# Optimization experiments

Hardware: AMD Instinct MI355X
Metric: run time of the kernel (lower is better)

## Reference

```python
import jax, jax.numpy as jnp
import numpy as np

D_MODEL, NHEAD, D_FF = 1024, 16, 4096
HEAD_DIM = D_MODEL // NHEAD
LN_EPS = 1e-5


def _layer_norm(x, g, b):
    m = jnp.mean(x, axis=-1, keepdims=True)
    v = jnp.var(x, axis=-1, keepdims=True)
    return (x - m) * jax.lax.rsqrt(v + LN_EPS) * g + b


def setup_inputs() -> dict:
    key = jax.random.key(0)
    ks = jax.random.split(key, 16)
    s = 0.02
    d = {
        "x": jax.random.normal(ks[0], (4, 2048, D_MODEL), dtype=jnp.float32),
        "wq": jax.random.normal(ks[1], (D_MODEL, D_MODEL), dtype=jnp.float32) * s,
        "bq": jnp.zeros((D_MODEL,), jnp.float32),
        "wk": jax.random.normal(ks[2], (D_MODEL, D_MODEL), dtype=jnp.float32) * s,
        "bk": jnp.zeros((D_MODEL,), jnp.float32),
        "wv": jax.random.normal(ks[3], (D_MODEL, D_MODEL), dtype=jnp.float32) * s,
        "bv": jnp.zeros((D_MODEL,), jnp.float32),
        "wo": jax.random.normal(ks[4], (D_MODEL, D_MODEL), dtype=jnp.float32) * s,
        "bo": jnp.zeros((D_MODEL,), jnp.float32),
        "ln1_g": jnp.ones((D_MODEL,), jnp.float32),
        "ln1_b": jnp.zeros((D_MODEL,), jnp.float32),
        "ln2_g": jnp.ones((D_MODEL,), jnp.float32),
        "ln2_b": jnp.zeros((D_MODEL,), jnp.float32),
        "w1": jax.random.normal(ks[5], (D_MODEL, D_FF), dtype=jnp.float32) * s,
        "b1": jnp.zeros((D_FF,), jnp.float32),
        "w2": jax.random.normal(ks[6], (D_FF, D_MODEL), dtype=jnp.float32) * s,
        "b2": jnp.zeros((D_MODEL,), jnp.float32),
        "wlr": jax.random.normal(ks[7], (D_MODEL, 1), dtype=jnp.float32) * s,
        "blr": jnp.zeros((1,), jnp.float32),
    }
    return d


def reference(x, wq, bq, wk, bk, wv, bv, wo, bo, ln1_g, ln1_b, ln2_g, ln2_b,
              w1, b1, w2, b2, wlr, blr):
    N, L, E = x.shape
    h, hd = NHEAD, HEAD_DIM

    # --- pre-LN self-attention ---
    xn = _layer_norm(x, ln1_g, ln1_b)
    q = (xn @ wq + bq).reshape(N, L, h, hd)
    k = (xn @ wk + bk).reshape(N, L, h, hd)
    v = (xn @ wv + bv).reshape(N, L, h, hd)
    scale = 1.0 / np.sqrt(hd).astype(np.float32)
    scores = jnp.einsum("nlhd,nshd->nhls", q, k) * scale  # [N,h,L,S]
    w = jax.nn.softmax(scores, axis=-1)
    attn = jnp.einsum("nhls,nshd->nlhd", w, v).reshape(N, L, E)
    x = x + (attn @ wo + bo)

    # --- pre-LN MLP (ReLU), dropout = identity in eval ---
    xn2 = _layer_norm(x, ln2_g, ln2_b)
    x = x + (jax.nn.relu(xn2 @ w1 + b1) @ w2 + b2)

    logits = x[:, 0] @ wlr + blr  # [N,1]
    half = logits.shape[0] // 2
    real, fake = logits[:half], logits[half:]
    # BCE-with-logits: target 1 -> softplus(-z); target 0 -> softplus(z)
    loss_real = jnp.mean(jax.nn.softplus(-real))
    loss_fake = jnp.mean(jax.nn.softplus(fake))
    loss = (loss_fake + loss_real) * 0.5
    return (x, loss, loss_fake)
```

## Files before the change

### kernel.cpp

```cpp
#include <hip/hip_runtime.h>

typedef float  float4v  __attribute__((ext_vector_type(4)));
typedef int    int4v    __attribute__((ext_vector_type(4)));
typedef unsigned short ushort4v __attribute__((ext_vector_type(4)));
typedef short  short4v  __attribute__((ext_vector_type(4)));
typedef __bf16 bf16x8   __attribute__((ext_vector_type(8)));
typedef __bf16 bf16x2   __attribute__((ext_vector_type(2)));

#define D_MODEL 1024
#define NHEAD   16
#define HEAD_DIM 64
#define D_FF    4096
#define SEQ     2048
#define NBATCH  4
#define NTOK    (SEQ*NBATCH)
#define QSTR    3072

#define SCL 0.18033688011112042f

__device__ __forceinline__ unsigned short f2bf(float f){
  __bf16 h = (__bf16)f;
  return __builtin_bit_cast(unsigned short, h);
}
__device__ __forceinline__ float bf2f(unsigned short h){
  unsigned int u = ((unsigned int)h) << 16;
  return __builtin_bit_cast(float, u);
}
__device__ __forceinline__ unsigned int pk2bf(float lo, float hi){
  bf16x2 v; v[0] = (__bf16)lo; v[1] = (__bf16)hi;
  return __builtin_bit_cast(unsigned int, v);
}

typedef const __attribute__((address_space(1))) void* as1cv;
typedef __attribute__((address_space(3))) void* as3v;
__device__ __forceinline__ void gl_lds16(const void* g, void* l){
  __builtin_amdgcn_global_load_lds((as1cv)(unsigned long long)g,
                                   (as3v)(unsigned int)(unsigned long long)l,
                                   16, 0, 0);
}

__global__ __launch_bounds__(256)
void transpose_bf16_k(const float* __restrict__ in, unsigned short* __restrict__ out,
                      int K, int N)
{
  __shared__ float t[32][33];
  const int n0 = blockIdx.x * 32, k0 = blockIdx.y * 32;
  const int tx = threadIdx.x & 31, ty = threadIdx.x >> 5;
  #pragma unroll
  for(int i=0;i<32;i+=8) t[ty+i][tx] = in[(long)(k0+ty+i)*N + n0 + tx];
  __syncthreads();
  #pragma unroll
  for(int i=0;i<32;i+=8) out[(long)(n0+ty+i)*K + k0 + tx] = f2bf(t[tx][ty+i]);
}

__global__ __launch_bounds__(256)
void concat_bias(const float* __restrict__ bq, const float* __restrict__ bk,
                 const float* __restrict__ bv, float* __restrict__ out)
{
  int i = blockIdx.x*256 + threadIdx.x;
  float v = (i < 1024) ? bq[i] : (i < 2048) ? bk[i-1024] : bv[i-2048];
  out[i] = v;
}

__global__ __launch_bounds__(256)
void transpose_v_head(const unsigned short* __restrict__ in,
                      unsigned short* __restrict__ out)
{
  __shared__ unsigned short t[64][72];
  const int s0 = blockIdx.x * 64, h = blockIdx.y, n = blockIdx.z;
  const int tid = threadIdx.x;
  #pragma unroll
  for(int i=0;i<2;i++){
    int id = i*256 + tid;
    int r = id >> 3, p = (id & 7) * 8;
    *(int4v*)&t[r][p] = *(const int4v*)&in[((long)(n*SEQ + s0 + r))*QSTR + h*HEAD_DIM + p];
  }
  __syncthreads();
  #pragma unroll
  for(int i=0;i<2;i++){
    int id = i*256 + tid;
    int d = id >> 3, p = (id & 7) * 8;
    ushort4v a, b;
    #pragma unroll
    for(int j=0;j<4;j++){ a[j] = t[p+j][d]; b[j] = t[p+4+j][d]; }
    unsigned short* dst = out + ((long)((n*NHEAD + h)*HEAD_DIM + d))*SEQ + s0 + p;
    *(ushort4v*)dst = a;
    *(ushort4v*)(dst+4) = b;
  }
}

__global__ __launch_bounds__(256)
void ln_bf16(const float* __restrict__ x, const float* __restrict__ g,
             const float* __restrict__ b, unsigned short* __restrict__ out)
{
  const int row = blockIdx.x, tid = threadIdx.x;
  const float* xr = x + (long)row * D_MODEL;
  float4v v = *(const float4v*)(xr + tid*4);
  float s = v[0]+v[1]+v[2]+v[3];
  float q = v[0]*v[0]+v[1]*v[1]+v[2]*v[2]+v[3]*v[3];
  #pragma unroll
  for(int off=32; off; off>>=1){ s += __shfl_down(s, off); q += __shfl_down(q, off); }
  __shared__ float sb[4], qb[4], stat[2];
  const int w = tid>>6, lane = tid&63;
  if(lane==0){ sb[w]=s; qb[w]=q; }
  __syncthreads();
  if(tid==0){
    float S = sb[0]+sb[1]+sb[2]+sb[3];
    float Q = qb[0]+qb[1]+qb[2]+qb[3];
    float mean = S * (1.0f/D_MODEL);
    float var  = Q * (1.0f/D_MODEL) - mean*mean;
    stat[0] = mean;
    stat[1] = rsqrtf(var + 1e-5f);
  }
  __syncthreads();
  const float mean = stat[0], rstd = stat[1];
  ushort4v o;
  #pragma unroll
  for(int i=0;i<4;i++){
    int c = tid*4 + i;
    o[i] = f2bf((v[i]-mean)*rstd*g[c] + b[c]);
  }
  *(ushort4v*)(out + (long)row*D_MODEL + tid*4) = o;
}

template<int EPI>
__global__ __launch_bounds__(256, 2)
void gemm_bf16(const unsigned short* __restrict__ A,
               const unsigned short* __restrict__ Bt,
               const float* __restrict__ bias,
               const float* __restrict__ res,
               void* __restrict__ Cout,
               int M, int N, int K)
{
  __shared__ unsigned short As[128][64];
  __shared__ unsigned short Bs[128][64];
  const int tid = threadIdx.x;
  const int bm = blockIdx.x, bn = blockIdx.y;
  const int lane = tid & 63, w = tid >> 6;
  const int wm = (w >> 1) * 64, wn = (w & 1) * 64;
  const int l15 = lane & 15, quad = lane >> 4;
  const int r8 = lane >> 3, c8 = lane & 7;
  const int swc = c8 ^ r8;

  float4v acc[4][4];
  #pragma unroll
  for(int i=0;i<4;i++)
    #pragma unroll
    for(int j=0;j<4;j++){ float4v z = {0.f,0.f,0.f,0.f}; acc[i][j] = z; }

  const unsigned short* Abase = A  + ((long)bm*128 + w*32 + r8)*K + swc*8;
  const unsigned short* Bbase = Bt + ((long)bn*128 + w*32 + r8)*K + swc*8;
  unsigned short* AsW = &As[w*32][0];
  unsigned short* BsW = &Bs[w*32][0];

  for(int k0 = 0; k0 < K; k0 += 64){
    __syncthreads();
    #pragma unroll
    for(int i=0;i<4;i++){
      gl_lds16(Abase + (long)i*8*K + k0, AsW + i*8*64);
      gl_lds16(Bbase + (long)i*8*K + k0, BsW + i*8*64);
    }
    __syncthreads();

    #pragma unroll
    for(int kh=0; kh<2; kh++){
      const int jsw = ((kh*4 + quad) ^ (l15 & 7)) * 8;
      bf16x8 af[4], bfr[4];
      #pragma unroll
      for(int i=0;i<4;i++){
        af[i]  = *(const bf16x8*)&As[wm + i*16 + l15][jsw];
        bfr[i] = *(const bf16x8*)&Bs[wn + i*16 + l15][jsw];
      }
      #pragma unroll
      for(int i=0;i<4;i++)
        #pragma unroll
        for(int j=0;j<4;j++)
          acc[i][j] = __builtin_amdgcn_mfma_f32_16x16x32_bf16(af[i], bfr[j], acc[i][j], 0, 0, 0);
    }
  }

  #pragma unroll
  for(int i=0;i<4;i++){
    #pragma unroll
    for(int r=0;r<4;r++){
      const int row = bm*128 + wm + i*16 + quad*4 + r;
      const long base = (long)row * N + bn*128 + wn;
      #pragma unroll
      for(int j=0;j<4;j++){
        const int ct = j*16 + l15;
        float val = acc[i][j][r] + bias[bn*128 + wn + ct];
        if constexpr (EPI == 1) val = fmaxf(val, 0.f);
        if constexpr (EPI == 2)
          ((float*)Cout)[base + ct] = val + res[base + ct];
        else
          ((unsigned short*)Cout)[base + ct] = f2bf(val);
      }
    }
  }
}

__global__ __launch_bounds__(256)
void attn_mfma(const unsigned short* __restrict__ qm,
               const unsigned short* __restrict__ km,
               const unsigned short* __restrict__ vt,
               unsigned short* __restrict__ om)
{
  __shared__ unsigned short Ks[2][128][64];
  __shared__ unsigned short Vs[2][64][128];

  const int tid = threadIdx.x;
  const int w = tid >> 6, lane = tid & 63;
  const int l15 = lane & 15, quad = lane >> 4;
  const int r8 = lane >> 3, c8 = lane & 7;
  const int swc = c8 ^ r8;
  const int h = blockIdx.y, n = blockIdx.z;
  const int qbase = blockIdx.x * 128 + w * 32;

  bf16x8 qf[2][2];
  #pragma unroll
  for(int g=0; g<2; g++)
    #pragma unroll
    for(int ds=0; ds<2; ds++)
      qf[g][ds] = *(const bf16x8*)(qm + ((long)(n*SEQ + qbase + g*16 + l15))*QSTR
                                      + h*HEAD_DIM + ds*32 + quad*8);

  const unsigned short* kstage = km + ((long)(n*SEQ + w*32 + r8))*QSTR + h*HEAD_DIM + swc*8;
  const unsigned short* vhead = vt + ((long)((n*NHEAD + h)*HEAD_DIM))*SEQ;
  const int vrow_off = (lane >> 4);
  const int vpos = lane & 15;

  float lsum[2] = {0.f, 0.f};
  float4v oacc[4][2];
  #pragma unroll
  for(int dt=0; dt<4; dt++)
    #pragma unroll
    for(int g=0; g<2; g++){ float4v z={0.f,0.f,0.f,0.f}; oacc[dt][g]=z; }

  {
    unsigned short* KsW = &Ks[0][w*32][0];
    #pragma unroll
    for(int i=0;i<4;i++)
      gl_lds16(kstage + (long)i*8*QSTR, KsW + i*8*64);
    #pragma unroll
    for(int i=0;i<4;i++){
      int vrow = w*16 + i*4 + vrow_off;
      gl_lds16(vhead + (long)vrow*SEQ + (vpos ^ (vrow & 7))*8,
               &Vs[0][w*16 + i*4][0]);
    }
  }
  __syncthreads();

  const int NT = SEQ/128;
  for(int t = 0; t < NT; t++){
    const int cur = t & 1;
    if(t + 1 < NT){
      const int s1 = (t+1)*128;
      unsigned short* KsW = &Ks[cur^1][w*32][0];
      const unsigned short* kn = kstage + (long)s1*QSTR;
      #pragma unroll
      for(int i=0;i<4;i++)
        gl_lds16(kn + (long)i*8*QSTR, KsW + i*8*64);
      #pragma unroll
      for(int i=0;i<4;i++){
        int vrow = w*16 + i*4 + vrow_off;
        gl_lds16(vhead + (long)vrow*SEQ + s1 + (vpos ^ (vrow & 7))*8,
                 &Vs[cur^1][w*16 + i*4][0]);
      }
    }

    #pragma unroll
    for(int c=0; c<8; c++){
      bf16x8 ka0 = *(const bf16x8*)&Ks[cur][c*16 + l15][((quad  ) ^ (l15 & 7))*8];
      bf16x8 ka1 = *(const bf16x8*)&Ks[cur][c*16 + l15][((quad+4) ^ (l15 & 7))*8];
      float4v s0a = {0.f,0.f,0.f,0.f}, s1a = {0.f,0.f,0.f,0.f};
      s0a = __builtin_amdgcn_mfma_f32_16x16x32_bf16(ka0, qf[0][0], s0a, 0,0,0);
      s0a = __builtin_amdgcn_mfma_f32_16x16x32_bf16(ka1, qf[0][1], s0a, 0,0,0);
      s1a = __builtin_amdgcn_mfma_f32_16x16x32_bf16(ka0, qf[1][0], s1a, 0,0,0);
      s1a = __builtin_amdgcn_mfma_f32_16x16x32_bf16(ka1, qf[1][1], s1a, 0,0,0);

      float p00 = exp2f(s0a[0]*SCL), p01 = exp2f(s0a[1]*SCL);
      float p02 = exp2f(s0a[2]*SCL), p03 = exp2f(s0a[3]*SCL);
      float p10 = exp2f(s1a[0]*SCL), p11 = exp2f(s1a[1]*SCL);
      float p12 = exp2f(s1a[2]*SCL), p13 = exp2f(s1a[3]*SCL);
      lsum[0] += (p00+p01)+(p02+p03);
      lsum[1] += (p10+p11)+(p12+p13);
      unsigned int pl0 = pk2bf(p00,p01), ph0 = pk2bf(p02,p03);
      unsigned int pl1 = pk2bf(p10,p11), ph1 = pk2bf(p12,p13);
      short4v pf0, pf1;
      pf0 = __builtin_bit_cast(short4v, (unsigned long long)pl0 | ((unsigned long long)ph0<<32));
      pf1 = __builtin_bit_cast(short4v, (unsigned long long)pl1 | ((unsigned long long)ph1<<32));

      const int cc = c*4 + quad;
      const int vcol = (((cc>>1) ^ (l15 & 7))*8 + (cc & 1)*4);
      #pragma unroll
      for(int dt=0; dt<4; dt++){
        ushort4v vu = *(const ushort4v*)&Vs[cur][dt*16 + l15][vcol];
        short4v vfr = __builtin_bit_cast(short4v, vu);
        oacc[dt][0] = __builtin_amdgcn_mfma_f32_16x16x16bf16_1k(vfr, pf0, oacc[dt][0], 0,0,0);
        oacc[dt][1] = __builtin_amdgcn_mfma_f32_16x16x16bf16_1k(vfr, pf1, oacc[dt][1], 0,0,0);
      }
    }
    __syncthreads();
  }

  #pragma unroll
  for(int g=0; g<2; g++){
    lsum[g] += __shfl_xor(lsum[g], 16);
    lsum[g] += __shfl_xor(lsum[g], 32);
  }
  float inv[2] = {1.f/lsum[0], 1.f/lsum[1]};

  unsigned short* Os = (unsigned short*)Ks + w*32*80;
  #pragma unroll
  for(int g=0; g<2; g++){
    #pragma unroll
    for(int dt=0; dt<4; dt++){
      unsigned int d0 = pk2bf(oacc[dt][g][0]*inv[g], oacc[dt][g][1]*inv[g]);
      unsigned int d1 = pk2bf(oacc[dt][g][2]*inv[g], oacc[dt][g][3]*inv[g]);
      unsigned int* dst = (unsigned int*)&Os[(g*16 + l15)*80 + dt*16 + quad*4];
      dst[0] = d0; dst[1] = d1;
    }
  }
  const int q = lane >> 1, half = lane & 1;
  unsigned short* orow = om + ((long)(n*SEQ + qbase + q))*D_MODEL + h*HEAD_DIM + half*32;
  #pragma unroll
  for(int j=0;j<4;j++){
    int4v vI = *(int4v*)&Os[q*80 + half*32 + j*8];
    *(int4v*)(orow + j*8) = vI;
  }
}

__global__ __launch_bounds__(256)
void loss_k(const float* __restrict__ xo, const float* __restrict__ wlr,
            const float* __restrict__ blr, float* __restrict__ out)
{
  const int tid = threadIdx.x, w = tid>>6, lane = tid&63;
  const float* row = xo + (long)w * SEQ * D_MODEL;
  float s = 0.f;
  for(int c=lane; c<D_MODEL; c+=64) s += row[c]*wlr[c];
  #pragma unroll
  for(int off=32; off; off>>=1) s += __shfl_down(s, off);
  __shared__ float lg[4];
  if(lane==0) lg[w] = s + blr[0];
  __syncthreads();
  if(tid==0){
    auto sp = [](float t){ return fmaxf(t, 0.f) + log1pf(__expf(-fabsf(t))); };
    float loss_real = 0.5f*(sp(-lg[0]) + sp(-lg[1]));
    float loss_fake = 0.5f*(sp( lg[2]) + sp( lg[3]));
    out[0] = 0.5f*(loss_fake + loss_real);
    out[1] = loss_fake;
  }
}

extern "C" void kernel_launch(void* const* d_in, const int* in_sizes, int n_in,
                              void* d_out, int out_size, void* d_ws, size_t ws_size,
                              hipStream_t stream)
{
  const float* x    = (const float*)d_in[0];
  const float* wq   = (const float*)d_in[1];
  const float* bq   = (const float*)d_in[2];
  const float* wk   = (const float*)d_in[3];
  const float* bk   = (const float*)d_in[4];
  const float* wv   = (const float*)d_in[5];
  const float* bv   = (const float*)d_in[6];
  const float* wo   = (const float*)d_in[7];
  const float* bo   = (const float*)d_in[8];
  const float* ln1g = (const float*)d_in[9];
  const float* ln1b = (const float*)d_in[10];
  const float* ln2g = (const float*)d_in[11];
  const float* ln2b = (const float*)d_in[12];
  const float* w1   = (const float*)d_in[13];
  const float* b1   = (const float*)d_in[14];
  const float* w2   = (const float*)d_in[15];
  const float* b2   = (const float*)d_in[16];
  const float* wlr  = (const float*)d_in[17];
  const float* blr  = (const float*)d_in[18];
  float* xout = (float*)d_out;

  char* ws = (char*)d_ws;
  unsigned short* xn     = (unsigned short*)(ws + (size_t)(  0<<20));
  unsigned short* wqkv_t = (unsigned short*)(ws + (size_t)( 16<<20));
  unsigned short* wo_t   = (unsigned short*)(ws + (size_t)( 22<<20));
  unsigned short* w1_t   = (unsigned short*)(ws + (size_t)( 24<<20));
  unsigned short* w2_t   = (unsigned short*)(ws + (size_t)( 32<<20));
  unsigned short* qkv    = (unsigned short*)(ws + (size_t)( 40<<20));
  unsigned short* attn   = (unsigned short*)(ws + (size_t)( 88<<20));
  unsigned short* vt     = (unsigned short*)(ws + (size_t)(104<<20));
  float*          bqkv   = (float*)         (ws + (size_t)(120<<20));
  unsigned short* hid    = (unsigned short*)(ws + (size_t)( 40<<20));

  dim3 blk(256);

  transpose_bf16_k<<<dim3(32,32),  blk, 0, stream>>>(wq, wqkv_t,               1024, 1024);
  transpose_bf16_k<<<dim3(32,32),  blk, 0, stream>>>(wk, wqkv_t + 1024*1024,   1024, 1024);
  transpose_bf16_k<<<dim3(32,32),  blk, 0, stream>>>(wv, wqkv_t + 2*1024*1024, 1024, 1024);
  transpose_bf16_k<<<dim3(32,32),  blk, 0, stream>>>(wo, wo_t, 1024, 1024);
  transpose_bf16_k<<<dim3(128,32), blk, 0, stream>>>(w1, w1_t, 1024, 4096);
  transpose_bf16_k<<<dim3(32,128), blk, 0, stream>>>(w2, w2_t, 4096, 1024);
  concat_bias<<<12, blk, 0, stream>>>(bq, bk, bv, bqkv);

  ln_bf16<<<NTOK, blk, 0, stream>>>(x, ln1g, ln1b, xn);

  gemm_bf16<0><<<dim3(64,24), blk, 0, stream>>>(xn, wqkv_t, bqkv, nullptr, qkv, NTOK, QSTR, 1024);

  transpose_v_head<<<dim3(SEQ/64, NHEAD, NBATCH), blk, 0, stream>>>(qkv + 2048, vt);

  attn_mfma<<<dim3(SEQ/128, NHEAD, NBATCH), blk, 0, stream>>>(qkv, qkv + 1024, vt, attn);

  gemm_bf16<2><<<dim3(64,8),  blk, 0, stream>>>(attn, wo_t, bo, x, xout, NTOK, 1024, 1024);

  ln_bf16<<<NTOK, blk, 0, stream>>>(xout, ln2g, ln2b, xn);

  gemm_bf16<1><<<dim3(64,32), blk, 0, stream>>>(xn,  w1_t, b1, nullptr, hid, NTOK, D_FF, 1024);
  gemm_bf16<2><<<dim3(64,8),  blk, 0, stream>>>(hid, w2_t, b2, xout, xout,   NTOK, 1024, D_FF);

  loss_k<<<1, blk, 0, stream>>>(xout, wlr, blr, xout + (size_t)NTOK*D_MODEL);
}
```

Baseline: 533.3 us.

## Fold softmax scale into Q projection and widen attention blocks to 8 waves

The QKV GEMM epilogue now multiplies the Q columns (bn<8) by the log2e-scaled softmax factor, so the attention loop can drop a multiply per score before exp2. The attention kernel moves from 256 to 512 threads, with each block covering 256 queries, so every K/V tile staged into LDS is reused by twice as many waves and each wave issues half as many global-to-LDS loads. The row sums are kept as vector accumulators and reduced once at the end. The trade-off is half as many attention blocks (512 instead of 1024), larger blocks that may lower occupancy, and rounding Q to bf16 after scaling rather than before.

After: 503.8 us. 1.06x faster.

```diff
diff --git a/kernel.cpp b/kernel.cpp
--- a/kernel.cpp
+++ b/kernel.cpp
@@ -190,6 +190,7 @@
         const int ct = j*16 + l15;
         float val = acc[i][j][r] + bias[bn*128 + wn + ct];
         if constexpr (EPI == 1) val = fmaxf(val, 0.f);
+        if constexpr (EPI == 3) { if(bn < 8) val *= SCL; }
         if constexpr (EPI == 2)
           ((float*)Cout)[base + ct] = val + res[base + ct];
         else
@@ -199,7 +200,7 @@
   }
 }
 
-__global__ __launch_bounds__(256)
+__global__ __launch_bounds__(512)
 void attn_mfma(const unsigned short* __restrict__ qm,
                const unsigned short* __restrict__ km,
                const unsigned short* __restrict__ vt,
@@ -214,7 +215,7 @@
   const int r8 = lane >> 3, c8 = lane & 7;
   const int swc = c8 ^ r8;
   const int h = blockIdx.y, n = blockIdx.z;
-  const int qbase = blockIdx.x * 128 + w * 32;
+  const int qbase = blockIdx.x * 256 + w * 32;
 
   bf16x8 qf[2][2];
   #pragma unroll
@@ -224,12 +225,12 @@
       qf[g][ds] = *(const bf16x8*)(qm + ((long)(n*SEQ + qbase + g*16 + l15))*QSTR
                                       + h*HEAD_DIM + ds*32 + quad*8);
 
-  const unsigned short* kstage = km + ((long)(n*SEQ + w*32 + r8))*QSTR + h*HEAD_DIM + swc*8;
+  const unsigned short* kstage = km + ((long)(n*SEQ + w*16 + r8))*QSTR + h*HEAD_DIM + swc*8;
   const unsigned short* vhead = vt + ((long)((n*NHEAD + h)*HEAD_DIM))*SEQ;
-  const int vrow_off = (lane >> 4);
-  const int vpos = lane & 15;
-
-  float lsum[2] = {0.f, 0.f};
+  const int vrow0 = w*8 + (lane >> 4);
+  const int vpos  = lane & 15;
+
+  float4v lsum4[2] = {{0.f,0.f,0.f,0.f},{0.f,0.f,0.f,0.f}};
   float4v oacc[4][2];
   #pragma unroll
   for(int dt=0; dt<4; dt++)
@@ -237,15 +238,14 @@
     for(int g=0; g<2; g++){ float4v z={0.f,0.f,0.f,0.f}; oacc[dt][g]=z; }
 
   {
-    unsigned short* KsW = &Ks[0][w*32][0];
-    #pragma unroll
-    for(int i=0;i<4;i++)
-      gl_lds16(kstage + (long)i*8*QSTR, KsW + i*8*64);
-    #pragma unroll
-    for(int i=0;i<4;i++){
-      int vrow = w*16 + i*4 + vrow_off;
+    #pragma unroll
+    for(int i=0;i<2;i++)
+      gl_lds16(kstage + (long)i*8*QSTR, &Ks[0][w*16 + i*8][0]);
+    #pragma unroll
+    for(int i=0;i<2;i++){
+      int vrow = vrow0 + i*4;
       gl_lds16(vhead + (long)vrow*SEQ + (vpos ^ (vrow & 7))*8,
-               &Vs[0][w*16 + i*4][0]);
+               &Vs[0][w*8 + i*4][0]);
     }
   }
   __syncthreads();
@@ -255,16 +255,15 @@
     const int cur = t & 1;
     if(t + 1 < NT){
       const int s1 = (t+1)*128;
-      unsigned short* KsW = &Ks[cur^1][w*32][0];
       const unsigned short* kn = kstage + (long)s1*QSTR;
       #pragma unroll
-      for(int i=0;i<4;i++)
-        gl_lds16(kn + (long)i*8*QSTR, KsW + i*8*64);
-      #pragma unroll
-      for(int i=0;i<4;i++){
-        int vrow = w*16 + i*4 + vrow_off;
+      for(int i=0;i<2;i++)
+        gl_lds16(kn + (long)i*8*QSTR, &Ks[cur^1][w*16 + i*8][0]);
+      #pragma unroll
+      for(int i=0;i<2;i++){
+        int vrow = vrow0 + i*4;
         gl_lds16(vhead + (long)vrow*SEQ + s1 + (vpos ^ (vrow & 7))*8,
-                 &Vs[cur^1][w*16 + i*4][0]);
+                 &Vs[cur^1][w*8 + i*4][0]);
       }
     }
 
@@ -278,12 +277,14 @@
       s1a = __builtin_amdgcn_mfma_f32_16x16x32_bf16(ka0, qf[1][0], s1a, 0,0,0);
       s1a = __builtin_amdgcn_mfma_f32_16x16x32_bf16(ka1, qf[1][1], s1a, 0,0,0);
 
-      float p00 = exp2f(s0a[0]*SCL), p01 = exp2f(s0a[1]*SCL);
-      float p02 = exp2f(s0a[2]*SCL), p03 = exp2f(s0a[3]*SCL);
-      float p10 = exp2f(s1a[0]*SCL), p11 = exp2f(s1a[1]*SCL);
-      float p12 = exp2f(s1a[2]*SCL), p13 = exp2f(s1a[3]*SCL);
-      lsum[0] += (p00+p01)+(p02+p03);
-      lsum[1] += (p10+p11)+(p12+p13);
+      float p00 = exp2f(s0a[0]), p01 = exp2f(s0a[1]);
+      float p02 = exp2f(s0a[2]), p03 = exp2f(s0a[3]);
+      float p10 = exp2f(s1a[0]), p11 = exp2f(s1a[1]);
+      float p12 = exp2f(s1a[2]), p13 = exp2f(s1a[3]);
+      float4v pv0 = {p00,p01,p02,p03};
+      float4v pv1 = {p10,p11,p12,p13};
+      lsum4[0] += pv0;
+      lsum4[1] += pv1;
       unsigned int pl0 = pk2bf(p00,p01), ph0 = pk2bf(p02,p03);
       unsigned int pl1 = pk2bf(p10,p11), ph1 = pk2bf(p12,p13);
       short4v pf0, pf1;
@@ -303,12 +304,14 @@
     __syncthreads();
   }
 
+  float inv[2];
   #pragma unroll
   for(int g=0; g<2; g++){
-    lsum[g] += __shfl_xor(lsum[g], 16);
-    lsum[g] += __shfl_xor(lsum[g], 32);
-  }
-  float inv[2] = {1.f/lsum[0], 1.f/lsum[1]};
+    float ls = (lsum4[g][0]+lsum4[g][1]) + (lsum4[g][2]+lsum4[g][3]);
+    ls += __shfl_xor(ls, 16);
+    ls += __shfl_xor(ls, 32);
+    inv[g] = 1.f/ls;
+  }
 
   unsigned short* Os = (unsigned short*)Ks + w*32*80;
   #pragma unroll
@@ -401,11 +404,11 @@
 
   ln_bf16<<<NTOK, blk, 0, stream>>>(x, ln1g, ln1b, xn);
 
-  gemm_bf16<0><<<dim3(64,24), blk, 0, stream>>>(xn, wqkv_t, bqkv, nullptr, qkv, NTOK, QSTR, 1024);
+  gemm_bf16<3><<<dim3(64,24), blk, 0, stream>>>(xn, wqkv_t, bqkv, nullptr, qkv, NTOK, QSTR, 1024);
 
   transpose_v_head<<<dim3(SEQ/64, NHEAD, NBATCH), blk, 0, stream>>>(qkv + 2048, vt);
 
-  attn_mfma<<<dim3(SEQ/128, NHEAD, NBATCH), blk, 0, stream>>>(qkv, qkv + 1024, vt, attn);
+  attn_mfma<<<dim3(SEQ/256, NHEAD, NBATCH), dim3(512), 0, stream>>>(qkv, qkv + 1024, vt, attn);
 
   gemm_bf16<2><<<dim3(64,8),  blk, 0, stream>>>(attn, wo_t, bo, x, xout, NTOK, 1024, 1024);
 
```
